# Optimization experiments

Measured on AMD Instinct MI355X. Metric: run time of the kernel, lower is better.

Reference implementation:

```python
import jax, jax.numpy as jnp
import numpy as np

NB_CLASSES = 256
EMBEDDING_SIZE = 50
TOTAL_CHARS = 8_000_000
NUM_WORDS = 1_600_000


def setup_inputs() -> dict:
    key = jax.random.key(0)
    k1, k2, k3 = jax.random.split(key, 3)
    char_ids = jax.random.randint(k1, (TOTAL_CHARS,), 0, NB_CLASSES, dtype=jnp.int64 if jax.config.jax_enable_x64 else jnp.int32)
    segment_ids = jnp.sort(jax.random.randint(k2, (TOTAL_CHARS,), 0, NUM_WORDS, dtype=char_ids.dtype))
    embedding_table = jax.random.normal(k3, (NB_CLASSES, EMBEDDING_SIZE), dtype=jnp.float32)
    return {
        "char_ids": char_ids,
        "segment_ids": segment_ids,
        "num_words": NUM_WORDS,
        "embedding_table": embedding_table,
    }


def reference(char_ids, segment_ids, num_words, embedding_table):
    # Fused ragged gather + segment-mean: equivalent to, for each word,
    # mean over its characters of embedding_table[char].
    char_emb = embedding_table[char_ids]                      # [total_chars, E]
    sums = jax.ops.segment_sum(char_emb, segment_ids, num_segments=num_words)  # [num_words, E]
    counts = jax.ops.segment_sum(
        jnp.ones((char_ids.shape[0],), dtype=embedding_table.dtype),
        segment_ids, num_segments=num_words)                  # [num_words]
    counts = jnp.maximum(counts, 1.0)                         # guard empty words
    return sums / counts[:, None]                             # [num_words, E]
```

## Files before the change

### kernel.cpp

```cpp
#include <hip/hip_runtime.h>


#define NB 256
#define EMB 50
#define BLK 1024
#define WPB (BLK / 64)

__global__ __launch_bounds__(256) void seg_starts4(
    const int* __restrict__ seg, int* __restrict__ starts, int n, int nw) {
  int base = (blockIdx.x * blockDim.x + threadIdx.x) * 4;
  if (base >= n) return;
  int lim = n - base; if (lim > 4) lim = 4;
  int vals[4];
  if (lim == 4) {
    int4 v = *(const int4*)(seg + base);
    vals[0] = v.x; vals[1] = v.y; vals[2] = v.z; vals[3] = v.w;
  } else {
    for (int u = 0; u < lim; ++u) vals[u] = seg[base + u];
  }
  int prev = (base > 0) ? seg[base - 1] : -1;
  for (int u = 0; u < lim; ++u) {
    int cur = vals[u];
    for (int w = prev + 1; w <= cur; ++w) starts[w] = base + u;
    prev = cur;
  }
  if (base + lim == n) {
    for (int w = prev + 1; w <= nw; ++w) starts[w] = n;
  }
}

#define RFL(x) __builtin_amdgcn_readfirstlane(x)

__global__ __launch_bounds__(BLK) void word_mean_v4(
    const int* __restrict__ char_ids, const float* __restrict__ table,
    const int* __restrict__ starts, float* __restrict__ out, int num_words) {
  __shared__ __align__(16) float tab[NB * EMB];
  for (int idx = threadIdx.x; idx < NB * EMB / 4; idx += BLK)
    ((float4*)tab)[idx] = ((const float4*)table)[idx];
  __syncthreads();

  const int lane = threadIdx.x & 63;
  const int k    = (lane < EMB) ? lane : (EMB - 1);
  const int wid0 = RFL(blockIdx.x * WPB + (threadIdx.x >> 6));
  const int nwv  = gridDim.x * WPB;

  for (int w = wid0; w < num_words; w += nwv) {
    const int s = RFL(starts[w]);
    const int e = RFL(starts[w + 1]);
    float acc = 0.f;
    int i = s;

    for (; i + 8 <= e; i += 8) {
      int c0 = RFL(char_ids[i + 0]); int c1 = RFL(char_ids[i + 1]);
      int c2 = RFL(char_ids[i + 2]); int c3 = RFL(char_ids[i + 3]);
      int c4 = RFL(char_ids[i + 4]); int c5 = RFL(char_ids[i + 5]);
      int c6 = RFL(char_ids[i + 6]); int c7 = RFL(char_ids[i + 7]);
      acc += tab[c0 * EMB + k]; acc += tab[c1 * EMB + k];
      acc += tab[c2 * EMB + k]; acc += tab[c3 * EMB + k];
      acc += tab[c4 * EMB + k]; acc += tab[c5 * EMB + k];
      acc += tab[c6 * EMB + k]; acc += tab[c7 * EMB + k];
    }
    if (i + 4 <= e) {
      int c0 = RFL(char_ids[i + 0]); int c1 = RFL(char_ids[i + 1]);
      int c2 = RFL(char_ids[i + 2]); int c3 = RFL(char_ids[i + 3]);
      acc += tab[c0 * EMB + k]; acc += tab[c1 * EMB + k];
      acc += tab[c2 * EMB + k]; acc += tab[c3 * EMB + k];
      i += 4;
    }
    for (; i < e; ++i) {
      int c = RFL(char_ids[i]);
      acc += tab[c * EMB + k];
    }

    const int cnt = e - s;
    const float inv = (cnt > 0) ? (1.0f / (float)cnt) : 0.0f;
    if (lane < EMB) out[(size_t)w * EMB + lane] = acc * inv;
  }
}

__device__ __forceinline__ int lb(const int* __restrict__ seg, int n, int w) {
  int lo = 0, hi = n;
  while (lo < hi) { int m = (lo + hi) >> 1; if (seg[m] < w) lo = m + 1; else hi = m; }
  return lo;
}
__global__ __launch_bounds__(256) void word_mean_bs_kernel(
    const int* __restrict__ char_ids, const int* __restrict__ seg,
    const float* __restrict__ table, float* __restrict__ out, int n, int num_words) {
  int w = blockIdx.x * blockDim.x + threadIdx.x;
  if (w >= num_words) return;
  int s = lb(seg, n, w), e = lb(seg, n, w + 1);
  float ax[25], ay[25];
#pragma unroll
  for (int p = 0; p < 25; ++p) { ax[p] = 0.f; ay[p] = 0.f; }
  for (int i = s; i < e; ++i) {
    const float2* row = (const float2*)(table + char_ids[i] * EMB);
#pragma unroll
    for (int p = 0; p < 25; ++p) { float2 v = row[p]; ax[p] += v.x; ay[p] += v.y; }
  }
  int cnt = e - s;
  float inv = (cnt > 0) ? (1.0f / (float)cnt) : 0.0f;
  float2* orow = (float2*)(out + (size_t)w * EMB);
#pragma unroll
  for (int p = 0; p < 25; ++p) orow[p] = make_float2(ax[p] * inv, ay[p] * inv);
}

extern "C" void kernel_launch(void* const* d_in, const int* in_sizes, int n_in,
                              void* d_out, int out_size, void* d_ws, size_t ws_size,
                              hipStream_t stream) {
  const int*   char_ids = (const int*)d_in[0];
  const int*   seg      = (const int*)d_in[1];
  const float* table    = (const float*)d_in[3];
  float*       out      = (float*)d_out;

  const int n  = in_sizes[0];
  const int nw = out_size / EMB;

  if (ws_size >= (size_t)(nw + 1) * sizeof(int)) {
    int* starts = (int*)d_ws;
    int nchunk = (n + 3) / 4;
    seg_starts4<<<(nchunk + 255) / 256, 256, 0, stream>>>(seg, starts, n, nw);
    word_mean_v4<<<512, BLK, 0, stream>>>(char_ids, table, starts, out, nw);
  } else {
    word_mean_bs_kernel<<<(nw + 255) / 256, 256, 0, stream>>>(
        char_ids, seg, table, out, n, nw);
  }
}
```

Before: 556.4 us.

## Batch 16 words per wavefront and broadcast char ids via readlane

Each wavefront now handles a group of 16 consecutive words. It loads all the word start offsets in one vector load and streams char_ids in coalesced 64-wide windows held in registers. Individual ids are pulled out with readlane instead of a separate scalar load per character. This is meant to cut the many small dependent scalar loads per word and the per-word starts lookups. The cost is extra window-management branches and readlane overhead, plus coarser load balancing across words.

```diff
diff --git a/kernel.cpp b/kernel.cpp
--- a/kernel.cpp
+++ b/kernel.cpp
@@ -5,6 +5,9 @@
 #define EMB 50
 #define BLK 1024
 #define WPB (BLK / 64)
+#define WG 16
+
+#define RL(v, l) __builtin_amdgcn_readlane((v), (l))
 
 __global__ __launch_bounds__(256) void seg_starts4(
     const int* __restrict__ seg, int* __restrict__ starts, int n, int nw) {
@@ -29,52 +32,78 @@
   }
 }
 
-#define RFL(x) __builtin_amdgcn_readfirstlane(x)
-
-__global__ __launch_bounds__(BLK) void word_mean_v4(
+__global__ __launch_bounds__(BLK) void word_mean_v5(
     const int* __restrict__ char_ids, const float* __restrict__ table,
-    const int* __restrict__ starts, float* __restrict__ out, int num_words) {
+    const int* __restrict__ starts, float* __restrict__ out,
+    int num_words, int n) {
   __shared__ __align__(16) float tab[NB * EMB];
   for (int idx = threadIdx.x; idx < NB * EMB / 4; idx += BLK)
     ((float4*)tab)[idx] = ((const float4*)table)[idx];
   __syncthreads();
 
   const int lane = threadIdx.x & 63;
-  const int k    = (lane < EMB) ? lane : (EMB - 1);
-  const int wid0 = RFL(blockIdx.x * WPB + (threadIdx.x >> 6));
-  const int nwv  = gridDim.x * WPB;
+  const float* tabk = tab + ((lane < EMB) ? lane : 0);
 
-  for (int w = wid0; w < num_words; w += nwv) {
-    const int s = RFL(starts[w]);
-    const int e = RFL(starts[w + 1]);
-    float acc = 0.f;
-    int i = s;
+  const int ngroups = (num_words + WG - 1) / WG;
+  const int gstep = gridDim.x * WPB;
 
-    for (; i + 8 <= e; i += 8) {
-      int c0 = RFL(char_ids[i + 0]); int c1 = RFL(char_ids[i + 1]);
-      int c2 = RFL(char_ids[i + 2]); int c3 = RFL(char_ids[i + 3]);
-      int c4 = RFL(char_ids[i + 4]); int c5 = RFL(char_ids[i + 5]);
-      int c6 = RFL(char_ids[i + 6]); int c7 = RFL(char_ids[i + 7]);
-      acc += tab[c0 * EMB + k]; acc += tab[c1 * EMB + k];
-      acc += tab[c2 * EMB + k]; acc += tab[c3 * EMB + k];
-      acc += tab[c4 * EMB + k]; acc += tab[c5 * EMB + k];
-      acc += tab[c6 * EMB + k]; acc += tab[c7 * EMB + k];
+  for (int g = blockIdx.x * WPB + (threadIdx.x >> 6); g < ngroups; g += gstep) {
+    const int w0 = g * WG;
+    const int wlim = min(WG, num_words - w0);
+
+    int sv = starts[w0 + min(lane, wlim)];
+    int base = RL(sv, 0);
+    int i = base;
+
+    int cv0 = char_ids[min(base + lane, n - 1)];
+    int cv1 = char_ids[min(base + 64 + lane, n - 1)];
+
+    for (int j = 0; j < wlim; ++j) {
+      const int ej = RL(sv, j + 1);
+      const int cnt = ej - i;
+      float acc = 0.f;
+
+      while (i + 4 <= ej) {
+        int t = i - base;
+        if (t >= 64) {
+          base += 64; t -= 64; cv0 = cv1;
+          cv1 = char_ids[min(base + 64 + lane, n - 1)];
+        }
+        int c0, c1, c2, c3;
+        if (t <= 60) {
+          c0 = RL(cv0, t); c1 = RL(cv0, t + 1); c2 = RL(cv0, t + 2); c3 = RL(cv0, t + 3);
+        } else {
+          int t0 = t & 63, t1 = (t + 1) & 63, t2 = (t + 2) & 63, t3 = (t + 3) & 63;
+          c0 = (t     < 64) ? RL(cv0, t0) : RL(cv1, t0);
+          c1 = (t + 1 < 64) ? RL(cv0, t1) : RL(cv1, t1);
+          c2 = (t + 2 < 64) ? RL(cv0, t2) : RL(cv1, t2);
+          c3 = (t + 3 < 64) ? RL(cv0, t3) : RL(cv1, t3);
+        }
+        float v0 = tabk[c0 * EMB], v1 = tabk[c1 * EMB];
+        float v2 = tabk[c2 * EMB], v3 = tabk[c3 * EMB];
+        acc += v0; acc += v1; acc += v2; acc += v3;
+        i += 4;
+      }
+      if (i + 2 <= ej) {
+        int t = i - base;
+        if (t >= 64) { base += 64; t -= 64; cv0 = cv1; cv1 = char_ids[min(base + 64 + lane, n - 1)]; }
+        int t0 = t & 63, t1 = (t + 1) & 63;
+        int c0 = (t < 64) ? RL(cv0, t0) : RL(cv1, t0);
+        int c1 = (t + 1 < 64) ? RL(cv0, t1) : RL(cv1, t1);
+        float v0 = tabk[c0 * EMB], v1 = tabk[c1 * EMB];
+        acc += v0; acc += v1;
+        i += 2;
+      }
+      if (i < ej) {
+        int t = i - base;
+        if (t >= 64) { base += 64; t -= 64; cv0 = cv1; cv1 = char_ids[min(base + 64 + lane, n - 1)]; }
+        acc += tabk[RL(cv0, t) * EMB];
+        ++i;
+      }
+
+      float inv = (cnt > 0) ? (1.0f / (float)cnt) : 0.0f;
+      if (lane < EMB) out[(size_t)(w0 + j) * EMB + lane] = acc * inv;
     }
-    if (i + 4 <= e) {
-      int c0 = RFL(char_ids[i + 0]); int c1 = RFL(char_ids[i + 1]);
-      int c2 = RFL(char_ids[i + 2]); int c3 = RFL(char_ids[i + 3]);
-      acc += tab[c0 * EMB + k]; acc += tab[c1 * EMB + k];
-      acc += tab[c2 * EMB + k]; acc += tab[c3 * EMB + k];
-      i += 4;
-    }
-    for (; i < e; ++i) {
-      int c = RFL(char_ids[i]);
-      acc += tab[c * EMB + k];
-    }
-
-    const int cnt = e - s;
-    const float inv = (cnt > 0) ? (1.0f / (float)cnt) : 0.0f;
-    if (lane < EMB) out[(size_t)w * EMB + lane] = acc * inv;
   }
 }
 
@@ -119,7 +148,7 @@
     int* starts = (int*)d_ws;
     int nchunk = (n + 3) / 4;
     seg_starts4<<<(nchunk + 255) / 256, 256, 0, stream>>>(seg, starts, n, nw);
-    word_mean_v4<<<512, BLK, 0, stream>>>(char_ids, table, starts, out, nw);
+    word_mean_v5<<<512, BLK, 0, stream>>>(char_ids, table, starts, out, nw, n);
   } else {
     word_mean_bs_kernel<<<(nw + 255) / 256, 256, 0, stream>>>(
         char_ids, seg, table, out, n, nw);
```

After: 493.5 us. -11.3%, faster.
